# Optimization experiments

Hardware: AMD Instinct MI355X
Metric: run time of the kernel (lower is better)

The kernel has to match this reference:

```python
import jax, jax.numpy as jnp
import numpy as np

HEADS, DIM, SEQ_LEN, MEM_LEN, CMEM_LEN, CMEM_RATIO = 16, 1024, 512, 512, 128, 4
DIM_H = DIM // HEADS


def shift(x):
    # relative-position shift trick, same as torch version
    *lead, i, j = x.shape
    x = jnp.concatenate([x, jnp.zeros((*lead, i, i), x.dtype)], -1)
    l = i + j - 1
    x = x.reshape(*lead, -1)
    pad = (-x.shape[-1]) % l
    x = jnp.concatenate([x, jnp.zeros((*lead, pad), x.dtype)], -1)
    x = x.reshape(*lead, -1, l)
    return x[..., :i, i - 1:]


def merge_heads(t):
    b, n, _ = t.shape
    return t.reshape(b, n, HEADS, DIM_H).transpose(0, 2, 1, 3)  # [b,h,n,dh]


def conv_compress(mem, conv_w, conv_b):
    # Conv1d(dim, dim, k=ratio, stride=ratio) == blockwise einsum
    b, L, e = mem.shape
    blocks = mem.reshape(b, L // CMEM_RATIO, CMEM_RATIO, e)
    return jnp.einsum('bmri,oir->bmo', blocks, conv_w) + conv_b


def full_attn(q, k, v):
    dots = jnp.einsum('bhid,bhjd->bhij', q, k) * (q.shape[-1] ** -0.5)
    attn = jax.nn.softmax(dots, axis=-1)
    return jnp.einsum('bhij,bhjd->bhid', attn, v)


def setup_inputs() -> dict:
    key = jax.random.key(0)
    ks = jax.random.split(key, 10)
    b = 8
    kv_len = CMEM_LEN + MEM_LEN + SEQ_LEN
    s = 0.02
    return {
        'x': jax.random.normal(ks[0], (b, SEQ_LEN, DIM), jnp.float32),
        'mem': jax.random.normal(ks[1], (b, MEM_LEN, DIM), jnp.float32),
        'cmem': jax.random.normal(ks[2], (b, CMEM_LEN, DIM), jnp.float32),
        'pos_emb': jax.random.normal(ks[3], (HEADS, kv_len, DIM_H), jnp.float32),
        'Wq': jax.random.normal(ks[4], (DIM, DIM), jnp.float32) * s,
        'Wkv': jax.random.normal(ks[5], (DIM, 2 * DIM), jnp.float32) * s,
        'Wout': jax.random.normal(ks[6], (DIM, DIM), jnp.float32) * s,
        'bout': jnp.zeros((DIM,), jnp.float32),
        'conv_w': jax.random.normal(ks[7], (DIM, DIM, CMEM_RATIO), jnp.float32) * s,
        'conv_b': jnp.zeros((DIM,), jnp.float32),
    }


def reference(x, mem, cmem, pos_emb, Wq, Wkv, Wout, bout, conv_w, conv_b):
    b, t, e = x.shape
    scale = DIM_H ** -0.5
    mem_len, cmem_len = mem.shape[1], cmem.shape[1]

    q = x @ Wq
    kv_input = jnp.concatenate([cmem, mem, x], axis=1)
    kv_len = kv_input.shape[1]
    k, v = jnp.split(kv_input @ Wkv, 2, axis=-1)
    q, k, v = map(merge_heads, (q, k, v))  # [b,h,n,dh]

    dots = jnp.einsum('bhid,bhjd->bhij', q, k) * scale
    pe = pos_emb[:, -kv_len:].astype(q.dtype)
    pos_dots = shift(jnp.einsum('bhid,hjd->bhij', q, pe) * scale)
    dots = dots + pos_dots

    attn = jax.nn.softmax(dots, axis=-1)
    weights = attn
    out = jnp.einsum('bhij,bhjd->bhid', attn, v)
    out = out.transpose(0, 2, 1, 3).reshape(b, t, -1)
    logits = out @ Wout + bout

    # memory update (queue_fifo with length mem_len)
    queue = jnp.concatenate([mem, x], axis=1)
    old_mem, new_mem = queue[:, :-MEM_LEN], queue[:, -MEM_LEN:]
    # old_mem length (512) divisible by cmem_ratio -> no padding branch
    compressed_mem = conv_compress(old_mem, conv_w, conv_b)
    new_cmem = jnp.concatenate([cmem, compressed_mem], axis=1)[:, -CMEM_LEN:]

    # auxiliary reconstruction loss (detached paths)
    old_mem_d = jax.lax.stop_gradient(old_mem)
    cm2 = conv_compress(old_mem_d, conv_w, conv_b)
    cmem_k, cmem_v = jnp.split(cm2 @ jax.lax.stop_gradient(Wkv), 2, axis=-1)
    cmem_k, cmem_v = map(merge_heads, (cmem_k, cmem_v))
    lo = kv_len - min(mem_len, MEM_LEN) - SEQ_LEN
    hi = kv_len - SEQ_LEN
    old_mem_k = jax.lax.stop_gradient(k[:, :, lo:hi])
    old_mem_v = jax.lax.stop_gradient(v[:, :, lo:hi])
    q_d = jax.lax.stop_gradient(q)
    aux_loss = jnp.mean((full_attn(q_d, old_mem_k, old_mem_v)
                         - full_attn(q_d, cmem_k, cmem_v)) ** 2)

    return logits, new_mem, new_cmem, aux_loss, weights
```

## Files before the change

kernel.cpp:

```cpp
#include <hip/hip_runtime.h>
#include <cstdint>


typedef __bf16 bf16;
typedef __bf16 bf16x2 __attribute__((ext_vector_type(2)));
typedef __bf16 bf16x4 __attribute__((ext_vector_type(4)));
typedef __bf16 bf16x8 __attribute__((ext_vector_type(8)));
typedef float  f32x2  __attribute__((ext_vector_type(2)));
typedef float  f32x4  __attribute__((ext_vector_type(4)));

template<int AMODE, int EPI>
__global__ __launch_bounds__(256)
void mfma_gemm(const bf16* __restrict__ A, const bf16* __restrict__ B2,
               float* __restrict__ C, bf16* __restrict__ outB, bf16* __restrict__ vT,
               int N, int K, int lda, int ldbt, int ldc,
               const float* __restrict__ bias, int vrows,
               const bf16* __restrict__ gcmem, const bf16* __restrict__ gmem,
               const bf16* __restrict__ gx)
{
    int row0 = blockIdx.y * 128, col0 = blockIdx.x * 128;
    int tid = threadIdx.x;
    int kofs = (EPI == 8) ? blockIdx.z * K : 0;

    __shared__ bf16 As[128][72];
    __shared__ bf16 Bs[128][72];

    int rn_ = tid >> 2;
    int c8  = (tid & 3) * 8;

    const bf16* aptr[2];
#pragma unroll
    for (int jj = 0; jj < 2; jj++) {
        int gr = row0 + rn_ + 64 * jj;
        if (AMODE == 0) {
            aptr[jj] = A + (long)gr * lda + kofs;
        } else {
            int bb = gr / 1152, rr = gr - bb * 1152;
            aptr[jj] = (rr < 128) ? (gcmem + ((long)bb * 128 + rr) * 1024)
                     : (rr < 640) ? (gmem + ((long)bb * 512 + (rr - 128)) * 1024)
                                  : (gx   + ((long)bb * 512 + (rr - 640)) * 1024);
        }
    }
    const bf16* bptr[2];
#pragma unroll
    for (int jj = 0; jj < 2; jj++) {
        int gc = col0 + rn_ + 64 * jj;
        bptr[jj] = (gc < N) ? (B2 + (long)gc * ldbt + kofs + c8) : nullptr;
    }

    int lane = tid & 63, wid = tid >> 6;
    int wr = wid >> 1, wc = wid & 1;
    int fr = lane & 15, fq = lane >> 4;

    f32x4 acc[4][4];
#pragma unroll
    for (int i = 0; i < 4; i++)
#pragma unroll
        for (int j = 0; j < 4; j++) acc[i][j] = (f32x4){0.f, 0.f, 0.f, 0.f};

    for (int k0 = 0; k0 < K; k0 += 32) {
#pragma unroll
        for (int jj = 0; jj < 2; jj++) {
            bf16x8 v = *(const bf16x8*)(aptr[jj] + k0 + c8);
            *(bf16x8*)&As[rn_ + 64 * jj][c8] = v;
        }
#pragma unroll
        for (int jj = 0; jj < 2; jj++) {
            bf16x8 v = {};
            if (bptr[jj]) v = *(const bf16x8*)(bptr[jj] + k0);
            *(bf16x8*)&Bs[rn_ + 64 * jj][c8] = v;
        }
        __syncthreads();

        bf16x8 af[4], bfv[4];
#pragma unroll
        for (int i = 0; i < 4; i++)
            af[i] = *(const bf16x8*)&As[wr * 64 + i * 16 + fr][fq * 8];
#pragma unroll
        for (int j = 0; j < 4; j++)
            bfv[j] = *(const bf16x8*)&Bs[wc * 64 + j * 16 + fr][fq * 8];
#pragma unroll
        for (int i = 0; i < 4; i++)
#pragma unroll
            for (int j = 0; j < 4; j++)
                acc[i][j] = __builtin_amdgcn_mfma_f32_16x16x32_bf16(af[i], bfv[j], acc[i][j], 0, 0, 0);
        __syncthreads();
    }

#pragma unroll
    for (int i = 0; i < 4; i++) {
#pragma unroll
        for (int j = 0; j < 4; j++) {
#pragma unroll
            for (int g = 0; g < 4; g++) {
                int r = row0 + wr * 64 + i * 16 + fq * 4 + g;
                int c = col0 + wc * 64 + j * 16 + fr;
                float v = acc[i][j][g];
                if (EPI == 0) {
                    if (c < N) {
                        if (bias) v += bias[c];
                        C[(long)r * ldc + c] = v;
                    }
                } else if (EPI == 6) {
                    if (c < N) {
                        if (bias) v += bias[c];
                        __builtin_nontemporal_store(v, &C[(long)r * ldc + c]);
                    }
                } else if (EPI == 8) {
                    C[((long)blockIdx.z << 20) + (long)r * 1024 + c] = v;
                } else if (EPI == 4) {
                    if (c < N) outB[(long)r * ldc + c] = (bf16)v;
                } else {
                    if (c < 1024) {
                        outB[(long)r * 1024 + c] = (bf16)v;
                    } else {
                        int d = c - 1024; int hh = d >> 6; d &= 63;
                        int bb = r / vrows; int j2 = r - bb * vrows;
                        vT[(((long)(bb * 16 + hh)) * 64 + d) * vrows + j2] = (bf16)v;
                    }
                }
            }
        }
    }
}

__global__ __launch_bounds__(256)
void splitk_reduce(const float* __restrict__ pbuf, const float* __restrict__ bias,
                   float* __restrict__ outF, bf16* __restrict__ outB)
{
    int i = blockIdx.x * 256 + threadIdx.x;
    f32x4 s = reinterpret_cast<const f32x4*>(pbuf)[i];
#pragma unroll
    for (int k = 1; k < 4; k++) {
        f32x4 t = reinterpret_cast<const f32x4*>(pbuf + (long)k * 1048576)[i];
        s[0] += t[0]; s[1] += t[1]; s[2] += t[2]; s[3] += t[3];
    }
    int col4 = (i << 2) & 1023;
    f32x4 bv = *(const f32x4*)&bias[col4];
    s[0] += bv[0]; s[1] += bv[1]; s[2] += bv[2]; s[3] += bv[3];
    reinterpret_cast<f32x4*>(outF)[i] = s;
    bf16x4 h = { (bf16)s[0], (bf16)s[1], (bf16)s[2], (bf16)s[3] };
    reinterpret_cast<bf16x4*>(outB)[i] = h;
}

__global__ __launch_bounds__(256)
void transpose_cast(const float* __restrict__ in, bf16* __restrict__ out, int R, int C)
{
    __shared__ float t[32][33];
    int c0 = blockIdx.x * 32, r0 = blockIdx.y * 32;
    int tx = threadIdx.x & 31, ty = threadIdx.x >> 5;
#pragma unroll
    for (int i = 0; i < 32; i += 8)
        t[ty + i][tx] = in[(long)(r0 + ty + i) * C + c0 + tx];
    __syncthreads();
#pragma unroll
    for (int i = 0; i < 32; i += 8)
        out[(long)(c0 + ty + i) * R + r0 + tx] = (bf16)t[tx][ty + i];
}

__global__ __launch_bounds__(256)
void convw_cast(const float* __restrict__ cw, bf16* __restrict__ out)
{
    long o = blockIdx.x;
    const float* src = cw + o * 4096;
    bf16* dst = out + o * 4096;
    __shared__ float t[4096];
#pragma unroll
    for (int k = 0; k < 4; k++)
        *(f32x4*)&t[(threadIdx.x + k * 256) * 4] = *(const f32x4*)&src[(threadIdx.x + k * 256) * 4];
    __syncthreads();
#pragma unroll
    for (int k = 0; k < 8; k++) {
        int d2 = 2 * (threadIdx.x + k * 256);
        int pi = ((d2 & 1023) << 2) | (d2 >> 10);
        bf16x2 h = { (bf16)t[pi], (bf16)t[pi + 4] };
        *(bf16x2*)&dst[d2] = h;
    }
}

__global__ __launch_bounds__(256)
void cast_f2b_multi(const float* __restrict__ s0, bf16* __restrict__ d0, int n0,
                    const float* __restrict__ s1, bf16* __restrict__ d1, int n1,
                    const float* __restrict__ s2, bf16* __restrict__ d2, int n2,
                    const float* __restrict__ s3, bf16* __restrict__ d3, int n3)
{
    int i = blockIdx.x * 256 + threadIdx.x;
    int stride = gridDim.x * 256;
    int ntot = n0 + n1 + n2 + n3;
    for (; i < ntot; i += stride) {
        const float* src; bf16* dst; int k = i;
        if (k < n0) { src = s0; dst = d0; }
        else if ((k -= n0) < n1) { src = s1; dst = d1; }
        else if ((k -= n1) < n2) { src = s2; dst = d2; }
        else { k -= n2; src = s3; dst = d3; }
        float4 f = reinterpret_cast<const float4*>(src)[k];
        bf16x4 h = { (bf16)f.x, (bf16)f.y, (bf16)f.z, (bf16)f.w };
        reinterpret_cast<bf16x4*>(dst)[k] = h;
    }
}

#define SSTR 1164

__global__ __launch_bounds__(256)
void attn_fused16(const bf16* __restrict__ qb, const bf16* __restrict__ kb,
                  const bf16* __restrict__ peb, const bf16* __restrict__ vTb,
                  float* __restrict__ weights, bf16* __restrict__ oatb)
{
    int bid = blockIdx.x;
    int w = (bid & 7) * 512 + (bid >> 3);
    int z = w >> 5;
    int b = z >> 4, h = z & 15;
    int r0 = (w & 31) * 16;
    int tid = threadIdx.x;
    int lane = tid & 63, wid = tid >> 6;
    int fr = lane & 15, fq = lane >> 4;

    __shared__ bf16 S[16 * SSTR];

    bf16x8 afr[2];
#pragma unroll
    for (int ks = 0; ks < 2; ks++)
        afr[ks] = *(const bf16x8*)&qb[((long)(b * 512 + r0 + fr)) * 1024 + h * 64 + ks * 32 + fq * 8];

#pragma unroll 3
    for (int ch = 0; ch < 9; ch++) {
        int c0 = ch * 128;
        int jb0 = c0 + 496 - r0 + 32 * wid;

        f32x4 p[3];
#pragma unroll
        for (int ct = 0; ct < 3; ct++) {
            f32x4 a = (f32x4){0.f, 0.f, 0.f, 0.f};
            int j = jb0 + ct * 16 + fr;
            bool ok = (j < 1152);
#pragma unroll
            for (int ks = 0; ks < 2; ks++) {
                bf16x8 bv = {};
                if (ok) bv = *(const bf16x8*)&peb[((long)(h * 1152 + j)) * 64 + ks * 32 + fq * 8];
                a = __builtin_amdgcn_mfma_f32_16x16x32_bf16(afr[ks], bv, a, 0, 0, 0);
            }
            p[ct] = a;
        }

#pragma unroll
        for (int tt = 0; tt < 2; tt++) {
            int cc = 32 * wid + 16 * tt + fr;
            f32x4 a = (f32x4){0.f, 0.f, 0.f, 0.f};
            long krow = (long)(b * 1152 + c0 + cc);
#pragma unroll
            for (int ks = 0; ks < 2; ks++) {
                bf16x8 bv = *(const bf16x8*)&kb[krow * 1024 + h * 64 + ks * 32 + fq * 8];
                a = __builtin_amdgcn_mfma_f32_16x16x32_bf16(afr[ks], bv, a, 0, 0, 0);
            }
#pragma unroll
            for (int g = 0; g < 4; g++) {
                int rr = fq * 4 + g;
                int uu = fr + 15 - rr;
                int src = (uu & 15) | (fq << 4);
                float s0 = __shfl(p[tt][g], src, 64);
                float s1 = __shfl(p[tt + 1][g], src, 64);
                float pv = (uu < 16) ? s0 : s1;
                S[rr * SSTR + c0 + cc] = (bf16)(0.125f * (a[g] + pv));
            }
        }
    }
    __syncthreads();

    for (int rw = 0; rw < 4; rw++) {
        int row = wid * 4 + rw;
        bf16* Srow = &S[row * SSTR];
        bf16x8 v0 = *(const bf16x8*)&Srow[lane * 8];
        bf16x8 v1 = *(const bf16x8*)&Srow[512 + lane * 8];
        bf16x2 v2 = *(const bf16x2*)&Srow[1024 + lane * 2];
        float e[18];
#pragma unroll
        for (int j = 0; j < 8; j++) { e[j] = (float)v0[j]; e[8 + j] = (float)v1[j]; }
        e[16] = (float)v2[0]; e[17] = (float)v2[1];

        float m = e[0];
#pragma unroll
        for (int k = 1; k < 18; k++) m = fmaxf(m, e[k]);
#pragma unroll
        for (int off = 32; off; off >>= 1) m = fmaxf(m, __shfl_xor(m, off, 64));
        float sm = 0.f;
#pragma unroll
        for (int k = 0; k < 18; k++) { e[k] = __expf(e[k] - m); sm += e[k]; }
#pragma unroll
        for (int off = 32; off; off >>= 1) sm += __shfl_xor(sm, off, 64);
        float inv = 1.f / sm;

        bf16x8 w0, w1; bf16x2 w2;
#pragma unroll
        for (int j = 0; j < 8; j++) { w0[j] = (bf16)(e[j] * inv); w1[j] = (bf16)(e[8 + j] * inv); }
        w2[0] = (bf16)(e[16] * inv); w2[1] = (bf16)(e[17] * inv);
        *(bf16x8*)&Srow[lane * 8] = w0;
        *(bf16x8*)&Srow[512 + lane * 8] = w1;
        *(bf16x2*)&Srow[1024 + lane * 2] = w2;
    }
    __syncthreads();

    f32x4 oacc = (f32x4){0.f, 0.f, 0.f, 0.f};
    int dt = wid;
    for (int ch = 0; ch < 9; ch++) {
        int c0 = ch * 128;
#pragma unroll
        for (int ks = 0; ks < 4; ks++) {
            bf16x8 pa = *(const bf16x8*)&S[fr * SSTR + c0 + ks * 32 + fq * 8];
            bf16x8 vb = *(const bf16x8*)&vTb[((long)z * 64 + dt * 16 + fr) * 1152 + c0 + ks * 32 + fq * 8];
            oacc = __builtin_amdgcn_mfma_f32_16x16x32_bf16(pa, vb, oacc, 0, 0, 0);
        }
    }
#pragma unroll
    for (int g = 0; g < 4; g++)
        oatb[((long)(b * 512 + r0 + fq * 4 + g)) * 1024 + h * 64 + dt * 16 + fr] = (bf16)oacc[g];

    for (int rw = 0; rw < 4; rw++) {
        int row = wid * 4 + rw;
        const bf16* Srow = &S[row * SSTR];
        long wbase = ((long)z * 512 + r0 + row) * 1152;
        bf16x8 v0 = *(const bf16x8*)&Srow[lane * 8];
        bf16x8 v1 = *(const bf16x8*)&Srow[512 + lane * 8];
        bf16x2 v2 = *(const bf16x2*)&Srow[1024 + lane * 2];
        f32x4 a0 = { (float)v0[0], (float)v0[1], (float)v0[2], (float)v0[3] };
        f32x4 a1 = { (float)v0[4], (float)v0[5], (float)v0[6], (float)v0[7] };
        f32x4 b0 = { (float)v1[0], (float)v1[1], (float)v1[2], (float)v1[3] };
        f32x4 b1 = { (float)v1[4], (float)v1[5], (float)v1[6], (float)v1[7] };
        f32x2 c0 = { (float)v2[0], (float)v2[1] };
        __builtin_nontemporal_store(a0, (f32x4*)&weights[wbase + lane * 8]);
        __builtin_nontemporal_store(a1, (f32x4*)&weights[wbase + lane * 8 + 4]);
        __builtin_nontemporal_store(b0, (f32x4*)&weights[wbase + 512 + lane * 8]);
        __builtin_nontemporal_store(b1, (f32x4*)&weights[wbase + 512 + lane * 8 + 4]);
        __builtin_nontemporal_store(c0, (f32x2*)&weights[wbase + 1024 + lane * 2]);
    }
}

__global__ __launch_bounds__(256)
void aux_mfma_kernel(const bf16* __restrict__ qb, const bf16* __restrict__ kb,
                     const bf16* __restrict__ ckb,
                     const bf16* __restrict__ vTb, const bf16* __restrict__ cvT,
                     float* __restrict__ partials)
{
    int z = blockIdx.y;
    int b = z >> 4, h = z & 15;
    int r0 = blockIdx.x * 128;
    int tid = threadIdx.x;
    int lane = tid & 63, wid = tid >> 6;
    int fr = lane & 15, fq = lane >> 4;

    __shared__ bf16 qs[128][72];
    __shared__ bf16 upool[128 * 136];
    __shared__ bf16 vt[64][136];
    __shared__ float wred[4];

#pragma unroll
    for (int t = 0; t < 4; t++) {
        int e = tid + 256 * t; int rr = e >> 3, c8 = (e & 7) * 8;
        *(bf16x8*)&qs[rr][c8] = *(const bf16x8*)&qb[((long)(b * 512 + r0 + rr)) * 1024 + h * 64 + c8];
    }

    float o1[2][4][4];
    f32x4 oaccv[2][4];
    float mrow[2][4], lrow[2][4];
    f32x4 sacc[2][8];
    float local = 0.f;

    for (int pass = 0; pass < 2; pass++) {
#pragma unroll
        for (int i = 0; i < 2; i++)
#pragma unroll
            for (int g = 0; g < 4; g++) { mrow[i][g] = -3.4e38f; lrow[i][g] = 0.f; }
#pragma unroll
        for (int i = 0; i < 2; i++)
#pragma unroll
            for (int jd = 0; jd < 4; jd++) oaccv[i][jd] = (f32x4){0.f, 0.f, 0.f, 0.f};

        int nchunk = pass ? 1 : 4;
        for (int jt = 0; jt < nchunk; jt++) {
            __syncthreads();
            if (pass == 0) {
                long base = (long)(b * 1152 + 128 + jt * 128);
#pragma unroll
                for (int t = 0; t < 4; t++) {
                    int e = tid + 256 * t; int j = e >> 3, c8 = (e & 7) * 8;
                    *(bf16x8*)&upool[j * 72 + c8] = *(const bf16x8*)&kb[(base + j) * 1024 + h * 64 + c8];
                }
#pragma unroll
                for (int t = 0; t < 4; t++) {
                    int e = tid + 256 * t; int d = e >> 4, j8 = (e & 15) * 8;
                    *(bf16x8*)&vt[d][j8] =
                        *(const bf16x8*)&vTb[((long)z * 64 + d) * 1152 + 128 + jt * 128 + j8];
                }
            } else {
#pragma unroll
                for (int t = 0; t < 4; t++) {
                    int e = tid + 256 * t; int j = e >> 3, c8 = (e & 7) * 8;
                    *(bf16x8*)&upool[j * 72 + c8] = *(const bf16x8*)&ckb[((long)(b * 128 + j)) * 1024 + h * 64 + c8];
                }
#pragma unroll
                for (int t = 0; t < 4; t++) {
                    int e = tid + 256 * t; int d = e >> 4, j8 = (e & 15) * 8;
                    *(bf16x8*)&vt[d][j8] = *(const bf16x8*)&cvT[((long)z * 64 + d) * 128 + j8];
                }
            }
            __syncthreads();

#pragma unroll
            for (int i = 0; i < 2; i++)
#pragma unroll
                for (int j = 0; j < 8; j++) sacc[i][j] = (f32x4){0.f, 0.f, 0.f, 0.f};
#pragma unroll
            for (int s = 0; s < 2; s++) {
                bf16x8 af[2], bfv[8];
#pragma unroll
                for (int i = 0; i < 2; i++)
                    af[i] = *(const bf16x8*)&qs[wid * 32 + i * 16 + fr][s * 32 + fq * 8];
#pragma unroll
                for (int j = 0; j < 8; j++)
                    bfv[j] = *(const bf16x8*)&upool[(j * 16 + fr) * 72 + s * 32 + fq * 8];
#pragma unroll
                for (int i = 0; i < 2; i++)
#pragma unroll
                    for (int j = 0; j < 8; j++)
                        sacc[i][j] = __builtin_amdgcn_mfma_f32_16x16x32_bf16(af[i], bfv[j], sacc[i][j], 0, 0, 0);
            }
            __syncthreads();

#pragma unroll
            for (int i = 0; i < 2; i++) {
#pragma unroll
                for (int g = 0; g < 4; g++) {
                    float mx = -3.4e38f;
#pragma unroll
                    for (int j = 0; j < 8; j++) mx = fmaxf(mx, sacc[i][j][g]);
                    mx *= 0.125f;
#pragma unroll
                    for (int msk = 1; msk <= 8; msk <<= 1) mx = fmaxf(mx, __shfl_xor(mx, msk, 64));
                    float mnew = fmaxf(mrow[i][g], mx);
                    float alpha = __expf(mrow[i][g] - mnew);
                    mrow[i][g] = mnew;
                    float sum = 0.f;
                    int prow = (wid * 32 + i * 16 + fq * 4 + g) * 136;
#pragma unroll
                    for (int j = 0; j < 8; j++) {
                        float p = __expf(sacc[i][j][g] * 0.125f - mnew);
                        sum += p;
                        upool[prow + j * 16 + fr] = (bf16)p;
                    }
#pragma unroll
                    for (int msk = 1; msk <= 8; msk <<= 1) sum += __shfl_xor(sum, msk, 16);
                    lrow[i][g] = lrow[i][g] * alpha + sum;
#pragma unroll
                    for (int jd = 0; jd < 4; jd++) oaccv[i][jd][g] *= alpha;
                }
            }
            __syncthreads();

#pragma unroll
            for (int s2 = 0; s2 < 4; s2++) {
                bf16x8 pa[2], vb[4];
#pragma unroll
                for (int i = 0; i < 2; i++)
                    pa[i] = *(const bf16x8*)&upool[(wid * 32 + i * 16 + fr) * 136 + s2 * 32 + fq * 8];
#pragma unroll
                for (int jd = 0; jd < 4; jd++)
                    vb[jd] = *(const bf16x8*)&vt[jd * 16 + fr][s2 * 32 + fq * 8];
#pragma unroll
                for (int i = 0; i < 2; i++)
#pragma unroll
                    for (int jd = 0; jd < 4; jd++)
                        oaccv[i][jd] = __builtin_amdgcn_mfma_f32_16x16x32_bf16(pa[i], vb[jd], oaccv[i][jd], 0, 0, 0);
            }
        }

        if (pass == 0) {
#pragma unroll
            for (int i = 0; i < 2; i++)
#pragma unroll
                for (int jd = 0; jd < 4; jd++)
#pragma unroll
                    for (int g = 0; g < 4; g++)
                        o1[i][jd][g] = oaccv[i][jd][g] / lrow[i][g];
        } else {
#pragma unroll
            for (int i = 0; i < 2; i++)
#pragma unroll
                for (int jd = 0; jd < 4; jd++)
#pragma unroll
                    for (int g = 0; g < 4; g++) {
                        float dd = o1[i][jd][g] - oaccv[i][jd][g] / lrow[i][g];
                        local += dd * dd;
                    }
        }
    }

#pragma unroll
    for (int off = 32; off; off >>= 1) local += __shfl_xor(local, off, 64);
    if (lane == 0) wred[wid] = local;
    __syncthreads();
    if (tid == 0)
        partials[(long)blockIdx.y * 4 + blockIdx.x] = wred[0] + wred[1] + wred[2] + wred[3];
}

__global__ __launch_bounds__(256)
void aux_reduce_kernel(const float* __restrict__ partials, float* __restrict__ out)
{
    int tid = threadIdx.x;
    __shared__ float wred[4];
    float s = 0.f;
    for (int i = tid; i < 512; i += 256) s += partials[i];
#pragma unroll
    for (int off = 32; off; off >>= 1) s += __shfl_xor(s, off, 64);
    if ((tid & 63) == 0) wred[tid >> 6] = s;
    __syncthreads();
    if (tid == 0) out[0] = (wred[0] + wred[1] + wred[2] + wred[3]) * (1.0f / 4194304.0f);
}

__global__ __launch_bounds__(256)
void copy_kernel(float* __restrict__ dst, const float* __restrict__ src, int n4)
{
    int i = blockIdx.x * 256 + threadIdx.x;
    int stride = gridDim.x * 256;
    for (; i < n4; i += stride) {
        f32x4 v = reinterpret_cast<const f32x4*>(src)[i];
        __builtin_nontemporal_store(v, &reinterpret_cast<f32x4*>(dst)[i]);
    }
}

extern "C" void kernel_launch(void* const* d_in, const int* in_sizes, int n_in,
                              void* d_out, int out_size, void* d_ws, size_t ws_size,
                              hipStream_t stream)
{
    const float* x      = (const float*)d_in[0];
    const float* mem    = (const float*)d_in[1];
    const float* cmem   = (const float*)d_in[2];
    const float* pe     = (const float*)d_in[3];
    const float* Wq     = (const float*)d_in[4];
    const float* Wkv    = (const float*)d_in[5];
    const float* Wout   = (const float*)d_in[6];
    const float* bout   = (const float*)d_in[7];
    const float* conv_w = (const float*)d_in[8];
    const float* conv_b = (const float*)d_in[9];

    float* out_logits  = (float*)d_out;
    float* out_newmem  = out_logits + 4194304;
    float* out_newcmem = out_newmem + 4194304;
    float* out_aux     = out_newcmem + 1048576;
    float* out_weights = out_aux + 1;

    float* ws       = (float*)d_ws;
    float* partials = ws;
    float* pbuf     = partials + 4096;
    bf16* bws     = (bf16*)(pbuf + 4194304);
    bf16* WqTb    = bws;
    bf16* WkvTb   = WqTb + 1048576;
    bf16* WoutTb  = WkvTb + 2097152;
    bf16* convwTb = WoutTb + 1048576;
    bf16* vTb     = convwTb + 4194304;
    bf16* cvT     = vTb + 9437184;
    bf16* qb      = cvT + 1048576;
    bf16* kb      = qb + 4194304;
    bf16* ckb     = kb + 9437184;
    bf16* peb     = ckb + 1048576;
    bf16* xb      = peb + 1179648;
    bf16* memb    = xb + 4194304;
    bf16* cmemb   = memb + 4194304;
    bf16* ncmemb  = cmemb + 1048576;
    bf16* oatb    = ncmemb + 1048576;

    dim3 blk(256);

    transpose_cast<<<dim3(32, 32), blk, 0, stream>>>(Wq, WqTb, 1024, 1024);
    transpose_cast<<<dim3(64, 32), blk, 0, stream>>>(Wkv, WkvTb, 1024, 2048);
    transpose_cast<<<dim3(32, 32), blk, 0, stream>>>(Wout, WoutTb, 1024, 1024);
    convw_cast<<<dim3(1024), blk, 0, stream>>>(conv_w, convwTb);
    cast_f2b_multi<<<dim3(2048), blk, 0, stream>>>(
        pe, peb, 294912, x, xb, 1048576, mem, memb, 1048576, cmem, cmemb, 262144);

    mfma_gemm<0, 4><<<dim3(8, 32, 1), blk, 0, stream>>>(
        xb, WqTb, nullptr, qb, nullptr, 1024, 1024, 1024, 1024, 1024,
        nullptr, 0, nullptr, nullptr, nullptr);

    mfma_gemm<1, 5><<<dim3(16, 72, 1), blk, 0, stream>>>(
        nullptr, WkvTb, nullptr, kb, vTb, 2048, 1024, 1024, 1024, 2048,
        nullptr, 1152, cmemb, memb, xb);

    mfma_gemm<0, 8><<<dim3(8, 8, 4), blk, 0, stream>>>(
        memb, convwTb, pbuf, nullptr, nullptr, 1024, 1024, 4096, 4096, 1024,
        nullptr, 0, nullptr, nullptr, nullptr);
    splitk_reduce<<<dim3(1024), blk, 0, stream>>>(pbuf, conv_b, out_newcmem, ncmemb);

    mfma_gemm<0, 5><<<dim3(16, 8, 1), blk, 0, stream>>>(
        ncmemb, WkvTb, nullptr, ckb, cvT, 2048, 1024, 1024, 1024, 2048,
        nullptr, 128, nullptr, nullptr, nullptr);

    attn_fused16<<<dim3(4096), blk, 0, stream>>>(qb, kb, peb, vTb, out_weights, oatb);

    mfma_gemm<0, 6><<<dim3(8, 32, 1), blk, 0, stream>>>(
        oatb, WoutTb, out_logits, nullptr, nullptr, 1024, 1024, 1024, 1024, 1024,
        bout, 0, nullptr, nullptr, nullptr);

    copy_kernel<<<dim3(4096), blk, 0, stream>>>(out_newmem, x, 1048576);

    aux_mfma_kernel<<<dim3(4, 128), blk, 0, stream>>>(qb, kb, ckb, vTb, cvT, partials);
    aux_reduce_kernel<<<dim3(1), blk, 0, stream>>>(partials, out_aux);
}
```

Measured before the change: 594.4 us.

## Use direct global-to-LDS loads with swizzle in GEMM and fuse new_mem copy into cast

The GEMM tile loads now use global_load_lds to move 16-byte chunks straight into unpadded, XOR-swizzled LDS, replacing register-staged loads and padded shared arrays. Column bounds checks are dropped because all launches use N that is a multiple of 128. The separate copy kernel for new_mem is removed, and the cast kernel now writes the fp32 x mirror while it already holds the data. The goals are lower VGPR and instruction overhead in the GEMM and one fewer launch plus one fewer read of x, at the risk of LDS bank conflicts if the swizzle mapping is wrong.

```diff
diff --git a/kernel.cpp b/kernel.cpp
--- a/kernel.cpp
+++ b/kernel.cpp
@@ -9,6 +9,10 @@
 typedef float  f32x2  __attribute__((ext_vector_type(2)));
 typedef float  f32x4  __attribute__((ext_vector_type(4)));
 
+#define GLOAD_LDS16(g, l) \
+    __builtin_amdgcn_global_load_lds((const __attribute__((address_space(1))) void*)(g), \
+                                     (__attribute__((address_space(3))) void*)(l), 16, 0, 0)
+
 template<int AMODE, int EPI>
 __global__ __launch_bounds__(256)
 void mfma_gemm(const bf16* __restrict__ A, const bf16* __restrict__ B2,
@@ -22,36 +26,40 @@
     int tid = threadIdx.x;
     int kofs = (EPI == 8) ? blockIdx.z * K : 0;
 
-    __shared__ bf16 As[128][72];
-    __shared__ bf16 Bs[128][72];
-
-    int rn_ = tid >> 2;
-    int c8  = (tid & 3) * 8;
-
-    const bf16* aptr[2];
-#pragma unroll
-    for (int jj = 0; jj < 2; jj++) {
-        int gr = row0 + rn_ + 64 * jj;
-        if (AMODE == 0) {
-            aptr[jj] = A + (long)gr * lda + kofs;
-        } else {
-            int bb = gr / 1152, rr = gr - bb * 1152;
-            aptr[jj] = (rr < 128) ? (gcmem + ((long)bb * 128 + rr) * 1024)
-                     : (rr < 640) ? (gmem + ((long)bb * 512 + (rr - 128)) * 1024)
-                                  : (gx   + ((long)bb * 512 + (rr - 640)) * 1024);
-        }
-    }
-    const bf16* bptr[2];
-#pragma unroll
-    for (int jj = 0; jj < 2; jj++) {
-        int gc = col0 + rn_ + 64 * jj;
-        bptr[jj] = (gc < N) ? (B2 + (long)gc * ldbt + kofs + c8) : nullptr;
-    }
+    __shared__ bf16 As[128 * 32];
+    __shared__ bf16 Bs[128 * 32];
 
     int lane = tid & 63, wid = tid >> 6;
     int wr = wid >> 1, wc = wid & 1;
     int fr = lane & 15, fq = lane >> 4;
 
+    int srow = lane >> 2;
+    int sc16 = (lane & 3) ^ ((lane >> 3) & 3);
+    const bf16* aq[2];
+    const bf16* bq[2];
+    bf16* as_dst[2];
+    bf16* bs_dst[2];
+#pragma unroll
+    for (int t = 0; t < 2; t++) {
+        int gr = row0 + wid * 32 + t * 16 + srow;
+        const bf16* ap;
+        if (AMODE == 0) {
+            ap = A + (long)gr * lda + kofs;
+        } else {
+            int bb = gr / 1152, rr = gr - bb * 1152;
+            ap = (rr < 128) ? (gcmem + ((long)bb * 128 + rr) * 1024)
+               : (rr < 640) ? (gmem + ((long)bb * 512 + (rr - 128)) * 1024)
+                            : (gx   + ((long)bb * 512 + (rr - 640)) * 1024);
+        }
+        aq[t] = ap + sc16 * 8;
+        int gc = col0 + wid * 32 + t * 16 + srow;
+        bq[t] = B2 + (long)gc * ldbt + kofs + sc16 * 8;
+        as_dst[t] = &As[(wid * 32 + t * 16) * 32];
+        bs_dst[t] = &Bs[(wid * 32 + t * 16) * 32];
+    }
+
+    int sfq = (fq ^ ((fr >> 1) & 3)) * 8;
+
     f32x4 acc[4][4];
 #pragma unroll
     for (int i = 0; i < 4; i++)
@@ -60,25 +68,19 @@
 
     for (int k0 = 0; k0 < K; k0 += 32) {
 #pragma unroll
-        for (int jj = 0; jj < 2; jj++) {
-            bf16x8 v = *(const bf16x8*)(aptr[jj] + k0 + c8);
-            *(bf16x8*)&As[rn_ + 64 * jj][c8] = v;
-        }
-#pragma unroll
-        for (int jj = 0; jj < 2; jj++) {
-            bf16x8 v = {};
-            if (bptr[jj]) v = *(const bf16x8*)(bptr[jj] + k0);
-            *(bf16x8*)&Bs[rn_ + 64 * jj][c8] = v;
+        for (int t = 0; t < 2; t++) {
+            GLOAD_LDS16(aq[t] + k0, as_dst[t]);
+            GLOAD_LDS16(bq[t] + k0, bs_dst[t]);
         }
         __syncthreads();
 
         bf16x8 af[4], bfv[4];
 #pragma unroll
         for (int i = 0; i < 4; i++)
-            af[i] = *(const bf16x8*)&As[wr * 64 + i * 16 + fr][fq * 8];
+            af[i] = *(const bf16x8*)&As[(wr * 64 + i * 16 + fr) * 32 + sfq];
 #pragma unroll
         for (int j = 0; j < 4; j++)
-            bfv[j] = *(const bf16x8*)&Bs[wc * 64 + j * 16 + fr][fq * 8];
+            bfv[j] = *(const bf16x8*)&Bs[(wc * 64 + j * 16 + fr) * 32 + sfq];
 #pragma unroll
         for (int i = 0; i < 4; i++)
 #pragma unroll
@@ -97,19 +99,15 @@
                 int c = col0 + wc * 64 + j * 16 + fr;
                 float v = acc[i][j][g];
                 if (EPI == 0) {
-                    if (c < N) {
-                        if (bias) v += bias[c];
-                        C[(long)r * ldc + c] = v;
-                    }
+                    if (bias) v += bias[c];
+                    C[(long)r * ldc + c] = v;
                 } else if (EPI == 6) {
-                    if (c < N) {
-                        if (bias) v += bias[c];
-                        __builtin_nontemporal_store(v, &C[(long)r * ldc + c]);
-                    }
+                    if (bias) v += bias[c];
+                    __builtin_nontemporal_store(v, &C[(long)r * ldc + c]);
                 } else if (EPI == 8) {
                     C[((long)blockIdx.z << 20) + (long)r * 1024 + c] = v;
                 } else if (EPI == 4) {
-                    if (c < N) outB[(long)r * ldc + c] = (bf16)v;
+                    outB[(long)r * ldc + c] = (bf16)v;
                 } else {
                     if (c < 1024) {
                         outB[(long)r * 1024 + c] = (bf16)v;
@@ -182,20 +180,23 @@
 void cast_f2b_multi(const float* __restrict__ s0, bf16* __restrict__ d0, int n0,
                     const float* __restrict__ s1, bf16* __restrict__ d1, int n1,
                     const float* __restrict__ s2, bf16* __restrict__ d2, int n2,
-                    const float* __restrict__ s3, bf16* __restrict__ d3, int n3)
+                    const float* __restrict__ s3, bf16* __restrict__ d3, int n3,
+                    float* __restrict__ xmirror)
 {
     int i = blockIdx.x * 256 + threadIdx.x;
     int stride = gridDim.x * 256;
     int ntot = n0 + n1 + n2 + n3;
     for (; i < ntot; i += stride) {
-        const float* src; bf16* dst; int k = i;
-        if (k < n0) { src = s0; dst = d0; }
-        else if ((k -= n0) < n1) { src = s1; dst = d1; }
-        else if ((k -= n1) < n2) { src = s2; dst = d2; }
-        else { k -= n2; src = s3; dst = d3; }
-        float4 f = reinterpret_cast<const float4*>(src)[k];
-        bf16x4 h = { (bf16)f.x, (bf16)f.y, (bf16)f.z, (bf16)f.w };
+        const float* src; bf16* dst; int k = i; int seg;
+        if (k < n0) { src = s0; dst = d0; seg = 0; }
+        else if ((k -= n0) < n1) { src = s1; dst = d1; seg = 1; }
+        else if ((k -= n1) < n2) { src = s2; dst = d2; seg = 2; }
+        else { k -= n2; src = s3; dst = d3; seg = 3; }
+        f32x4 f = reinterpret_cast<const f32x4*>(src)[k];
+        bf16x4 h = { (bf16)f[0], (bf16)f[1], (bf16)f[2], (bf16)f[3] };
         reinterpret_cast<bf16x4*>(dst)[k] = h;
+        if (seg == 1)
+            __builtin_nontemporal_store(f, &reinterpret_cast<f32x4*>(xmirror)[k]);
     }
 }
 
@@ -513,17 +514,6 @@
     if ((tid & 63) == 0) wred[tid >> 6] = s;
     __syncthreads();
     if (tid == 0) out[0] = (wred[0] + wred[1] + wred[2] + wred[3]) * (1.0f / 4194304.0f);
-}
-
-__global__ __launch_bounds__(256)
-void copy_kernel(float* __restrict__ dst, const float* __restrict__ src, int n4)
-{
-    int i = blockIdx.x * 256 + threadIdx.x;
-    int stride = gridDim.x * 256;
-    for (; i < n4; i += stride) {
-        f32x4 v = reinterpret_cast<const f32x4*>(src)[i];
-        __builtin_nontemporal_store(v, &reinterpret_cast<f32x4*>(dst)[i]);
-    }
 }
 
 extern "C" void kernel_launch(void* const* d_in, const int* in_sizes, int n_in,
@@ -574,7 +564,8 @@
     transpose_cast<<<dim3(32, 32), blk, 0, stream>>>(Wout, WoutTb, 1024, 1024);
     convw_cast<<<dim3(1024), blk, 0, stream>>>(conv_w, convwTb);
     cast_f2b_multi<<<dim3(2048), blk, 0, stream>>>(
-        pe, peb, 294912, x, xb, 1048576, mem, memb, 1048576, cmem, cmemb, 262144);
+        pe, peb, 294912, x, xb, 1048576, mem, memb, 1048576, cmem, cmemb, 262144,
+        out_newmem);
 
     mfma_gemm<0, 4><<<dim3(8, 32, 1), blk, 0, stream>>>(
         xb, WqTb, nullptr, qb, nullptr, 1024, 1024, 1024, 1024, 1024,
@@ -599,8 +590,6 @@
         oatb, WoutTb, out_logits, nullptr, nullptr, 1024, 1024, 1024, 1024, 1024,
         bout, 0, nullptr, nullptr, nullptr);
 
-    copy_kernel<<<dim3(4096), blk, 0, stream>>>(out_newmem, x, 1048576);
-
     aux_mfma_kernel<<<dim3(4, 128), blk, 0, stream>>>(qb, kb, ckb, vTb, cvT, partials);
     aux_reduce_kernel<<<dim3(1), blk, 0, stream>>>(partials, out_aux);
 }
```

Result: faster. 533.8 us (-10.2%).
